# Kernel tuning notes

Hardware: AMD Instinct MI355X
Metric: run time of the kernel (lower is better)

The kernel has to match this reference:

```python
import jax, jax.numpy as jnp
import numpy as np

DIM, NH, HD = 1536, 12, 128
F, H, W = 1, 30, 52
SEQ = F * H * W          # 1560 tokens per AR group
NG, GI = 6, 5            # num_groups, group_idx (attend over full prefix)
POS, EPS = 1024, 1e-6


def _rope_table():
    # cos/sin table matching Wan rope_params: bands [c-2(c//3), c//3, c//3] of head_dim//2
    c = HD // 2
    parts = [c - 2 * (c // 3), c // 3, c // 3]
    pos = np.arange(POS, dtype=np.float64)
    angs = []
    for cp in parts:
        inv = 1.0 / (10000.0 ** (np.arange(cp, dtype=np.float64) / cp))
        angs.append(pos[:, None] * inv[None, :])
    ang = np.concatenate(angs, axis=1)  # [POS, c]
    return jnp.asarray(np.stack([np.cos(ang), np.sin(ang)], axis=-1), dtype=jnp.float32)


def setup_inputs() -> dict:
    key = jax.random.key(0)
    ks = jax.random.split(key, 8)
    lin = lambda k: jax.random.normal(k, (DIM, DIM), jnp.float32) * 0.02
    total = NG * SEQ
    return {
        'x': jax.random.normal(ks[0], (1, SEQ, DIM), jnp.float32),
        'wq': lin(ks[1]), 'bq': jnp.zeros((DIM,), jnp.float32),
        'wk': lin(ks[2]), 'bk': jnp.zeros((DIM,), jnp.float32),
        'wv': lin(ks[3]), 'bv': jnp.zeros((DIM,), jnp.float32),
        'wo': lin(ks[4]), 'bo': jnp.zeros((DIM,), jnp.float32),
        'nq_w': jnp.ones((DIM,), jnp.float32),
        'nk_w': jnp.ones((DIM,), jnp.float32),
        'freqs': _rope_table(),
        'k_cache': jax.random.normal(ks[5], (1, total, NH, HD), jnp.float32) * 0.5,
        'v_cache': jax.random.normal(ks[6], (1, total, NH, HD), jnp.float32) * 0.5,
        'f': F, 'h': H, 'w': W, 'group_idx': GI, 'num_groups': NG,
    }


def _rms_norm(x, weight, eps=EPS):
    # fast_rms_norm: normalize over the full channel dim, then scale
    x = x.astype(jnp.float32)
    return x * jax.lax.rsqrt(jnp.mean(x * x, axis=-1, keepdims=True) + eps) * weight


def _rope_apply(x, freqs, f, h, w, group_idx):
    # x: [B, S, N, D] with S = f*h*w; freqs: [POS, D//2, 2] (cos, sin)
    B, S, N, D = x.shape
    c = D // 2
    cf = c - 2 * (c // 3)
    ch = cw = c // 3
    sf = group_idx * f
    fp = jnp.broadcast_to(freqs[sf:sf + f, :cf][:, None, None], (f, h, w, cf, 2))
    hp = jnp.broadcast_to(freqs[:h, cf:cf + ch][None, :, None], (f, h, w, ch, 2))
    wp = jnp.broadcast_to(freqs[:w, cf + ch:][None, None, :], (f, h, w, cw, 2))
    rot = jnp.concatenate([fp, hp, wp], axis=3).reshape(S, c, 2)  # [S, c, 2]
    cos = rot[..., 0][None, :, None]  # [1, S, 1, c]
    sin = rot[..., 1][None, :, None]
    xr = x.astype(jnp.float32).reshape(B, S, N, c, 2)
    out_r = xr[..., 0] * cos - xr[..., 1] * sin  # complex multiply x * e^{i theta}
    out_i = xr[..., 0] * sin + xr[..., 1] * cos
    return jnp.stack([out_r, out_i], axis=-1).reshape(B, S, N, D)


def reference(x, wq, bq, wk, bk, wv, bv, wo, bo, nq_w, nk_w, freqs,
              k_cache, v_cache, f, h, w, group_idx, num_groups):
    B, S, C = x.shape
    n, d = NH, C // NH
    q = _rms_norm(x @ wq.T + bq, nq_w).reshape(B, S, n, d)
    k = _rms_norm(x @ wk.T + bk, nk_w).reshape(B, S, n, d)
    v = (x @ wv.T + bv).reshape(B, S, n, d)
    q = _rope_apply(q, freqs, f, h, w, group_idx)
    k = _rope_apply(k, freqs, f, h, w, group_idx)
    # KV-cache scatter (detached in the original) then prefix gather
    start = group_idx * S
    kc = jax.lax.dynamic_update_slice(k_cache, jax.lax.stop_gradient(k), (0, start, 0, 0))
    vc = jax.lax.dynamic_update_slice(v_cache, jax.lax.stop_gradient(v), (0, start, 0, 0))
    k_full = kc[:, :start + S]  # [B, Lkv, n, d]
    v_full = vc[:, :start + S]
    att = jnp.einsum('bqnd,bknd->bnqk', q, k_full) / jnp.sqrt(jnp.float32(d))
    p = jax.nn.softmax(att, axis=-1)
    o = jnp.einsum('bnqk,bknd->bqnd', p, v_full).reshape(B, S, C)
    return o @ wo.T + bo
```

## Files before the change

### kernel.cpp

```cpp
#include <hip/hip_runtime.h>

#define DIM 1536
#define NH 12
#define HD 128
#define KSPLIT 8
#define KT 32
#define MFIX 3.0f

typedef _Float16 half2_t __attribute__((ext_vector_type(2)));
typedef _Float16 half8_t __attribute__((ext_vector_type(8)));
typedef float f32x4 __attribute__((ext_vector_type(4)));

__device__ __forceinline__ half2_t pkrtz(float a, float b) {
    return __builtin_bit_cast(half2_t, __builtin_amdgcn_cvt_pkrtz(a, b));
}

__device__ __forceinline__ void split8(float4 a, float4 b, half8_t& h, half8_t& l) {
    half2_t h0 = pkrtz(a.x, a.y), h1 = pkrtz(a.z, a.w);
    half2_t h2 = pkrtz(b.x, b.y), h3 = pkrtz(b.z, b.w);
    half2_t g0 = pkrtz(a.x - (float)h0.x, a.y - (float)h0.y);
    half2_t g1 = pkrtz(a.z - (float)h1.x, a.w - (float)h1.y);
    half2_t g2 = pkrtz(b.x - (float)h2.x, b.y - (float)h2.y);
    half2_t g3 = pkrtz(b.z - (float)h3.x, b.w - (float)h3.y);
    h[0]=h0.x; h[1]=h0.y; h[2]=h1.x; h[3]=h1.y; h[4]=h2.x; h[5]=h2.y; h[6]=h3.x; h[7]=h3.y;
    l[0]=g0.x; l[1]=g0.y; l[2]=g1.x; l[3]=g1.y; l[4]=g2.x; l[5]=g2.y; l[6]=g3.x; l[7]=g3.y;
}

__device__ __forceinline__ half8_t cvt8rn(float4 a, float4 b) {
    half8_t h;
    h[0]=(_Float16)a.x; h[1]=(_Float16)a.y; h[2]=(_Float16)a.z; h[3]=(_Float16)a.w;
    h[4]=(_Float16)b.x; h[5]=(_Float16)b.y; h[6]=(_Float16)b.z; h[7]=(_Float16)b.w;
    return h;
}

__device__ __forceinline__ void gl2lds16(const void* g, void* l) {
    __builtin_amdgcn_global_load_lds(
        (const __attribute__((address_space(1))) unsigned int*)g,
        (__attribute__((address_space(3))) unsigned int*)(unsigned int)(uintptr_t)l,
        16, 0, 0);
}

__global__ __launch_bounds__(256) void cvt_hl(
    const float* __restrict__ src, _Float16* __restrict__ h, _Float16* __restrict__ l, int n8)
{
    const int i = blockIdx.x * 256 + threadIdx.x;
    if (i >= n8) return;
    const float4* s = (const float4*)src + (size_t)i * 2;
    float4 a = s[0], b = s[1];
    half8_t hh, ll; split8(a, b, hh, ll);
    ((half8_t*)h)[i] = hh;
    ((half8_t*)l)[i] = ll;
}

__global__ __launch_bounds__(256) void cvt_hl4(
    const float* __restrict__ s0, const float* __restrict__ s1,
    const float* __restrict__ s2, const float* __restrict__ s3,
    _Float16* __restrict__ h0, _Float16* __restrict__ l0,
    _Float16* __restrict__ h1, _Float16* __restrict__ l1,
    _Float16* __restrict__ h2, _Float16* __restrict__ l2,
    _Float16* __restrict__ h3, _Float16* __restrict__ l3, int n8)
{
    const int i = blockIdx.x * 256 + threadIdx.x;
    if (i >= n8) return;
    const int m = blockIdx.y;
    const float* src = m == 0 ? s0 : m == 1 ? s1 : m == 2 ? s2 : s3;
    _Float16* h = m == 0 ? h0 : m == 1 ? h1 : m == 2 ? h2 : h3;
    _Float16* l = m == 0 ? l0 : m == 1 ? l1 : m == 2 ? l2 : l3;
    const float4* s = (const float4*)src + (size_t)i * 2;
    float4 a = s[0], b = s[1];
    half8_t hh, ll; split8(a, b, hh, ll);
    ((half8_t*)h)[i] = hh;
    ((half8_t*)l)[i] = ll;
}

#define ASTR 40
__global__ __launch_bounds__(256) void gemm_f16_tn(
    const _Float16* __restrict__ Ah, const _Float16* __restrict__ Al,
    const _Float16* __restrict__ Bh0, const _Float16* __restrict__ Bl0,
    const _Float16* __restrict__ Bh1, const _Float16* __restrict__ Bl1,
    const _Float16* __restrict__ Bh2, const _Float16* __restrict__ Bl2,
    const float* __restrict__ bias0, const float* __restrict__ bias1, const float* __restrict__ bias2,
    float* __restrict__ C0, float* __restrict__ C1, float* __restrict__ C2,
    int M)
{
    __shared__ __align__(16) _Float16 AhL[128][ASTR], AlL[128][ASTR];
    __shared__ __align__(16) _Float16 BhL[128][ASTR], BlL[128][ASTR];
    const int bx = blockIdx.x, by = blockIdx.y;
    const int mat = bx / 12, nt = bx % 12;
    const _Float16* Bh   = mat == 0 ? Bh0 : mat == 1 ? Bh1 : Bh2;
    const _Float16* Bl   = mat == 0 ? Bl0 : mat == 1 ? Bl1 : Bl2;
    const float*    bias = mat == 0 ? bias0 : mat == 1 ? bias1 : bias2;
    float*          C    = mat == 0 ? C0 : mat == 1 ? C1 : C2;
    const int m0 = by * 128, n0 = nt * 128;
    const int tid = threadIdx.x;
    const int lane = tid & 63, wave = tid >> 6;
    const int l16 = lane & 15, quad = lane >> 4;
    const int wm = (wave >> 1) * 64, wn = (wave & 1) * 64;
    const int srow = tid >> 1;
    const int scol = (tid & 1) * 16;
    const bool avalid = (m0 + srow) < M;
    const _Float16* ahp = Ah + (size_t)(avalid ? m0 + srow : 0) * DIM + scol;
    const _Float16* alp = Al + (size_t)(avalid ? m0 + srow : 0) * DIM + scol;
    const _Float16* bhp = Bh + (size_t)(n0 + srow) * DIM + scol;
    const _Float16* blp = Bl + (size_t)(n0 + srow) * DIM + scol;

    f32x4 acc[4][4];
    #pragma unroll
    for (int i = 0; i < 4; ++i)
        #pragma unroll
        for (int j = 0; j < 4; ++j) acc[i][j] = (f32x4){0.f, 0.f, 0.f, 0.f};

    for (int kk = 0; kk < DIM; kk += 32) {
        __syncthreads();
        uint4 z = {0, 0, 0, 0};
        uint4 a0 = z, a1 = z, a2 = z, a3 = z;
        if (avalid) {
            a0 = *(const uint4*)(ahp + kk);
            a1 = *(const uint4*)(ahp + kk + 8);
            a2 = *(const uint4*)(alp + kk);
            a3 = *(const uint4*)(alp + kk + 8);
        }
        uint4 b0 = *(const uint4*)(bhp + kk);
        uint4 b1 = *(const uint4*)(bhp + kk + 8);
        uint4 b2 = *(const uint4*)(blp + kk);
        uint4 b3 = *(const uint4*)(blp + kk + 8);
        *(uint4*)&AhL[srow][scol]     = a0;
        *(uint4*)&AhL[srow][scol + 8] = a1;
        *(uint4*)&AlL[srow][scol]     = a2;
        *(uint4*)&AlL[srow][scol + 8] = a3;
        *(uint4*)&BhL[srow][scol]     = b0;
        *(uint4*)&BhL[srow][scol + 8] = b1;
        *(uint4*)&BlL[srow][scol]     = b2;
        *(uint4*)&BlL[srow][scol + 8] = b3;
        __syncthreads();
        half8_t ah[4], al[4], bh[4], bl[4];
        #pragma unroll
        for (int ms = 0; ms < 4; ++ms) {
            ah[ms] = *(const half8_t*)&AhL[wm + ms*16 + l16][quad*8];
            al[ms] = *(const half8_t*)&AlL[wm + ms*16 + l16][quad*8];
        }
        #pragma unroll
        for (int ns = 0; ns < 4; ++ns) {
            bh[ns] = *(const half8_t*)&BhL[wn + ns*16 + l16][quad*8];
            bl[ns] = *(const half8_t*)&BlL[wn + ns*16 + l16][quad*8];
        }
        #pragma unroll
        for (int ms = 0; ms < 4; ++ms)
            #pragma unroll
            for (int ns = 0; ns < 4; ++ns) {
                acc[ms][ns] = __builtin_amdgcn_mfma_f32_16x16x32_f16(ah[ms], bh[ns], acc[ms][ns], 0, 0, 0);
                acc[ms][ns] = __builtin_amdgcn_mfma_f32_16x16x32_f16(ah[ms], bl[ns], acc[ms][ns], 0, 0, 0);
                acc[ms][ns] = __builtin_amdgcn_mfma_f32_16x16x32_f16(al[ms], bh[ns], acc[ms][ns], 0, 0, 0);
            }
    }
    float bv[4];
    #pragma unroll
    for (int ns = 0; ns < 4; ++ns) bv[ns] = bias[n0 + wn + ns*16 + l16];
    #pragma unroll
    for (int ms = 0; ms < 4; ++ms)
        #pragma unroll
        for (int r = 0; r < 4; ++r) {
            const int row = m0 + wm + ms*16 + quad*4 + r;
            if (row < M) {
                #pragma unroll
                for (int ns = 0; ns < 4; ++ns)
                    C[(size_t)row * DIM + n0 + wn + ns*16 + l16] = acc[ms][ns][r] + bv[ns];
            }
        }
}

__global__ __launch_bounds__(256) void rms_rope2(
    float* __restrict__ qb, float* __restrict__ kb,
    const float* __restrict__ wq_, const float* __restrict__ wk_,
    const float* __restrict__ freqs,
    const int* __restrict__ fp, const int* __restrict__ hp,
    const int* __restrict__ wp, const int* __restrict__ gip)
{
    const int s = blockIdx.x;
    float* xv = blockIdx.y ? kb : qb;
    const float* w = blockIdx.y ? wk_ : wq_;
    const int tid = threadIdx.x;
    float* row = xv + (size_t)s * DIM;
    float ss = 0.f;
    for (int c = tid; c < DIM; c += 256) { float v = row[c]; ss += v * v; }
    #pragma unroll
    for (int off = 32; off > 0; off >>= 1) ss += __shfl_down(ss, off, 64);
    __shared__ float red[4];
    if ((tid & 63) == 0) red[tid >> 6] = ss;
    __syncthreads();
    const float tot = red[0] + red[1] + red[2] + red[3];
    const float scale = rsqrtf(tot / (float)DIM + 1e-6f);
    const int f = *fp, h = *hp, ww = *wp, gi = *gip;
    const int hw = h * ww;
    const int fi = s / hw;
    const int rem = s - fi * hw;
    const int hi = rem / ww;
    const int wi = rem - hi * ww;
    const int sf = gi * f;
    for (int p = tid; p < DIM / 2; p += 256) {
        int n = p >> 6, i = p & 63;
        int pos = (i < 22) ? (sf + fi) : (i < 43) ? hi : wi;
        float cs = freqs[pos * 128 + i * 2];
        float sn = freqs[pos * 128 + i * 2 + 1];
        int base = n * HD + 2 * i;
        float x0 = row[base] * scale * w[base];
        float x1 = row[base + 1] * scale * w[base + 1];
        row[base] = x0 * cs - x1 * sn;
        row[base + 1] = x0 * sn + x1 * cs;
    }
}

__global__ __launch_bounds__(256) void kv_prep(
    const float* __restrict__ kws, const float* __restrict__ kcache,
    const float* __restrict__ vws, const float* __restrict__ vcache,
    _Float16* __restrict__ KV, int S, int NT, const int* __restrict__ gip)
{
    const int t = blockIdx.x, n = blockIdx.y;
    const int tid = threadIdx.x;
    const int lane = tid & 63;
    const int l16 = lane & 15, quad = lane >> 4;
    const int start = gip[0] * S;
    const int nk = start + S;
    _Float16* outk = KV + (size_t)(n * NT + t) * 8192;
    _Float16* outv = outk + 4096;
    #pragma unroll
    for (int fi = 0; fi < 2; ++fi) {
        const int f = (tid >> 6) + fi * 4;
        const int ks = f >> 2, db = f & 3;
        const int j = t * KT + ks * 16 + l16;
        float4 a = make_float4(0,0,0,0), b = a;
        if (j < nk) {
            const float* src = (j < start) ? (kcache + (size_t)j * DIM)
                                           : (kws + (size_t)(j - start) * DIM);
            src += n * HD + db * 32 + quad * 8;
            a = *(const float4*)src;
            b = *(const float4*)(src + 4);
        }
        *(half8_t*)&outk[(f * 64 + lane) * 8] = cvt8rn(a, b);
    }
    #pragma unroll
    for (int fi = 0; fi < 2; ++fi) {
        const int ds = (tid >> 6) + fi * 4;
        const int dim = n * HD + ds * 16 + l16;
        half8_t h;
        #pragma unroll
        for (int j = 0; j < 8; ++j) {
            const int key = t * KT + quad * 8 + j;
            float v = 0.f;
            if (key < nk)
                v = (key < start) ? vcache[(size_t)key * DIM + dim]
                                  : vws[(size_t)(key - start) * DIM + dim];
            h[j] = (_Float16)v;
        }
        *(half8_t*)&outv[(ds * 64 + lane) * 8] = h;
    }
}

#define PSTRH 40
__global__ __launch_bounds__(512) void attn_mfma(
    const float* __restrict__ q,
    const _Float16* __restrict__ KV,
    float* __restrict__ Op, float* __restrict__ Ml,
    int S, int NT, const int* __restrict__ gip)
{
    __shared__ __align__(16) _Float16 T[2][8192];
    __shared__ __align__(16) _Float16 Ph[8][16][PSTRH];

    const int nwg = gridDim.x;
    const int L = blockIdx.x;
    const int q8 = nwg >> 3, r8 = nwg & 7;
    const int xcd = L & 7, si = L >> 3;
    const int logical = (xcd < r8 ? xcd * (q8 + 1)
                                  : r8 * (q8 + 1) + (xcd - r8) * q8) + si;
    const int yb = (S + 127) >> 7;
    const int y = logical % yb;
    const int g = logical / yb;
    const int n = g % NH;
    const int ksp = g / NH;
    const int q0 = y * 128;

    const int tid = threadIdx.x;
    const int wave = tid >> 6;
    const int lane = tid & 63;
    const int l16 = lane & 15;
    const int quad = lane >> 4;
    const int start = gip[0] * S;
    const int nk = start + S;
    const int totTiles = (nk + KT - 1) / KT;
    const int tilesPer = (totTiles + KSPLIT - 1) / KSPLIT;
    const int t0 = ksp * tilesPer;
    const int t1 = min(t0 + tilesPer, totTiles);
    const float sc = 0.08838834764831845f;

    half8_t qf[4];
    {
        const int qrow = q0 + wave * 16 + l16;
        const bool qv = qrow < S;
        const float* qp = q + (size_t)(qv ? qrow : 0) * DIM + n * HD + quad * 8;
        #pragma unroll
        for (int db = 0; db < 4; ++db) {
            float4 a = make_float4(0,0,0,0), b = a;
            if (qv) { a = *(const float4*)(qp + db * 32); b = *(const float4*)(qp + db * 32 + 4); }
            qf[db] = cvt8rn(a, b);
        }
    }

    half8_t ones_f;
    {
        _Float16 ov = (l16 == 0) ? (_Float16)1.0f : (_Float16)0.0f;
        #pragma unroll
        for (int j = 0; j < 8; ++j) ones_f[j] = ov;
    }

    f32x4 O[9];
    #pragma unroll
    for (int ds = 0; ds < 9; ++ds) O[ds] = (f32x4){0.f, 0.f, 0.f, 0.f};

    const size_t tb = (size_t)n * NT;

    if (t0 < t1) {
        const _Float16* gp = KV + (tb + t0) * 8192 + wave * 512 + lane * 8;
        gl2lds16(gp,        &T[0][wave * 512]);
        gl2lds16(gp + 4096, &T[0][wave * 512 + 4096]);
    }

    int cur = 0;
    for (int t = t0; t < t1; ++t) {
        if (t + 1 < t1) {
            const _Float16* gp = KV + (tb + t + 1) * 8192 + wave * 512 + lane * 8;
            _Float16* d = &T[cur ^ 1][wave * 512];
            gl2lds16(gp,        d);
            gl2lds16(gp + 4096, d + 4096);
            asm volatile("s_waitcnt vmcnt(2)" ::: "memory");
        } else {
            asm volatile("s_waitcnt vmcnt(0)" ::: "memory");
        }
        __builtin_amdgcn_s_barrier();
        __builtin_amdgcn_sched_barrier(0);

        f32x4 sacc[2];
        sacc[0] = (f32x4){0.f, 0.f, 0.f, 0.f};
        sacc[1] = (f32x4){0.f, 0.f, 0.f, 0.f};
        const half8_t* kh8 = (const half8_t*)&T[cur][0];
        __builtin_amdgcn_s_setprio(1);
        #pragma unroll
        for (int ks = 0; ks < 2; ++ks) {
            #pragma unroll
            for (int db = 0; db < 4; ++db) {
                half8_t bh = kh8[(ks * 4 + db) * 64 + lane];
                sacc[ks] = __builtin_amdgcn_mfma_f32_16x16x32_f16(qf[db], bh, sacc[ks], 0, 0, 0);
            }
        }
        __builtin_amdgcn_s_setprio(0);

        const int k0 = t * KT;
        const bool v0 = (k0 + l16) < nk;
        const bool v1 = (k0 + 16 + l16) < nk;
        #pragma unroll
        for (int r = 0; r < 4; ++r) {
            float p0 = v0 ? __expf(sacc[0][r] * sc - MFIX) : 0.f;
            float p1 = v1 ? __expf(sacc[1][r] * sc - MFIX) : 0.f;
            Ph[wave][quad * 4 + r][l16] = (_Float16)p0;
            Ph[wave][quad * 4 + r][16 + l16] = (_Float16)p1;
        }

        half8_t ph = *(const half8_t*)&Ph[wave][l16][quad * 8];

        const half8_t* vt8 = (const half8_t*)&T[cur][4096];
        __builtin_amdgcn_s_setprio(1);
        #pragma unroll
        for (int ds = 0; ds < 8; ++ds) {
            half8_t vh = vt8[ds * 64 + lane];
            O[ds] = __builtin_amdgcn_mfma_f32_16x16x32_f16(ph, vh, O[ds], 0, 0, 0);
        }
        O[8] = __builtin_amdgcn_mfma_f32_16x16x32_f16(ph, ones_f, O[8], 0, 0, 0);
        __builtin_amdgcn_s_setprio(0);

        __builtin_amdgcn_sched_barrier(0);
        __builtin_amdgcn_s_barrier();
        cur ^= 1;
    }

    #pragma unroll
    for (int r = 0; r < 4; ++r) {
        const int row = q0 + wave * 16 + quad * 4 + r;
        if (row < S) {
            float* op = Op + (((size_t)ksp * NH + n) * S + row) * HD + l16;
            #pragma unroll
            for (int ds = 0; ds < 8; ++ds) op[ds * 16] = O[ds][r];
            if (l16 == 0)
                Ml[((size_t)ksp * NH + n) * S + row] = O[8][r];
        }
    }
}

__global__ __launch_bounds__(256) void attn_merge(
    const float* __restrict__ Op, const float* __restrict__ Ml,
    _Float16* __restrict__ oh, _Float16* __restrict__ ol, int S)
{
    const int idx = blockIdx.x * 256 + threadIdx.x;
    const int total = NH * S * HD / 2;
    if (idx >= total) return;
    const int d0 = (idx & 63) * 2;
    const int t = idx >> 6;
    const int row = t % S;
    const int n = t / S;
    float num0 = 0.f, num1 = 0.f, den = 0.f;
    #pragma unroll
    for (int ks = 0; ks < KSPLIT; ++ks) {
        const size_t base = ((size_t)ks * NH + n) * S + row;
        num0 += Op[base * HD + d0];
        num1 += Op[base * HD + d0 + 1];
        den += Ml[base];
    }
    const float v0 = num0 / den, v1 = num1 / den;
    half2_t h = pkrtz(v0, v1);
    half2_t l = pkrtz(v0 - (float)h.x, v1 - (float)h.y);
    const size_t oidx = (size_t)row * DIM + n * HD + d0;
    *(half2_t*)&oh[oidx] = h;
    *(half2_t*)&ol[oidx] = l;
}

extern "C" void kernel_launch(void* const* d_in, const int* in_sizes, int n_in,
                              void* d_out, int out_size, void* d_ws, size_t ws_size,
                              hipStream_t stream)
{
    const float* x      = (const float*)d_in[0];
    const float* wq     = (const float*)d_in[1];
    const float* bq     = (const float*)d_in[2];
    const float* wk     = (const float*)d_in[3];
    const float* bk     = (const float*)d_in[4];
    const float* wv     = (const float*)d_in[5];
    const float* bv     = (const float*)d_in[6];
    const float* wo     = (const float*)d_in[7];
    const float* bo     = (const float*)d_in[8];
    const float* nqw    = (const float*)d_in[9];
    const float* nkw    = (const float*)d_in[10];
    const float* freqs  = (const float*)d_in[11];
    const float* kcache = (const float*)d_in[12];
    const float* vcache = (const float*)d_in[13];
    const int*   fp     = (const int*)d_in[14];
    const int*   hp     = (const int*)d_in[15];
    const int*   wp     = (const int*)d_in[16];
    const int*   gip    = (const int*)d_in[17];

    const int S = in_sizes[0] / DIM;
    const int total = in_sizes[12] / (NH * HD);
    const int NT = (total + KT - 1) / KT;
    const size_t sd = (size_t)S * DIM;
    const size_t wsz = (size_t)DIM * DIM;

    char* p = (char*)d_ws;
    float* q  = (float*)p;            p += sd * 4;
    float* k  = (float*)p;            p += sd * 4;
    float* v  = (float*)p;            p += sd * 4;
    float* Op = (float*)p;            p += (size_t)KSPLIT * NH * S * HD * 4;
    float* Ml = (float*)p;            p += (size_t)KSPLIT * NH * S * 4;
    _Float16* KV  = (_Float16*)p;     p += (size_t)NH * NT * 8192 * 2;
    _Float16* xh  = (_Float16*)p;     p += sd * 2;
    _Float16* xl  = (_Float16*)p;     p += sd * 2;
    _Float16* oh  = (_Float16*)p;     p += sd * 2;
    _Float16* ol  = (_Float16*)p;     p += sd * 2;
    _Float16* wqh = (_Float16*)p;     p += wsz * 2;
    _Float16* wql = (_Float16*)p;     p += wsz * 2;
    _Float16* wkh = (_Float16*)p;     p += wsz * 2;
    _Float16* wkl = (_Float16*)p;     p += wsz * 2;
    _Float16* wvh = (_Float16*)p;     p += wsz * 2;
    _Float16* wvl = (_Float16*)p;     p += wsz * 2;
    _Float16* woh = (_Float16*)p;     p += wsz * 2;
    _Float16* wol = (_Float16*)p;     p += wsz * 2;
    float* out = (float*)d_out;

    const int mt = (S + 127) / 128;
    const int xn8 = (int)(sd / 8), wn8 = (int)(wsz / 8);

    cvt_hl<<<dim3((xn8 + 255) / 256), dim3(256), 0, stream>>>(x, xh, xl, xn8);
    cvt_hl4<<<dim3((wn8 + 255) / 256, 4), dim3(256), 0, stream>>>(
        wq, wk, wv, wo, wqh, wql, wkh, wkl, wvh, wvl, woh, wol, wn8);

    gemm_f16_tn<<<dim3(36, mt), dim3(256), 0, stream>>>(
        xh, xl, wqh, wql, wkh, wkl, wvh, wvl, bq, bk, bv, q, k, v, S);
    rms_rope2<<<dim3(S, 2), dim3(256), 0, stream>>>(q, k, nqw, nkw, freqs, fp, hp, wp, gip);
    kv_prep<<<dim3(NT, NH), dim3(256), 0, stream>>>(k, kcache, v, vcache, KV, S, NT, gip);
    {
        const int yb = (S + 127) / 128;
        const int nwg = NH * yb * KSPLIT;
        attn_mfma<<<dim3(nwg), dim3(512), 0, stream>>>(
            q, KV, Op, Ml, S, NT, gip);
    }
    attn_merge<<<dim3((NH * S * HD / 2 + 255) / 256), dim3(256), 0, stream>>>(Op, Ml, oh, ol, S);
    gemm_f16_tn<<<dim3(12, mt), dim3(256), 0, stream>>>(
        oh, ol, woh, wol, woh, wol, woh, wol, bo, bo, bo, out, out, out, S);
}
```

Measured before the change: 518.3 us.

## Pre-tile GEMM operands into MFMA fragment layout with async double-buffered LDS loads

The fp16 hi/lo conversion kernels and the attention merge now write activations and weights in a tiled, fragment-ordered layout, one 4096-element record per 128x32 tile. The GEMM can then stage each tile with direct global-to-LDS 16-byte loads, double-buffered with explicit vmcnt waits and raw barriers, and read fragments from LDS without padding. Blocks are also remapped across XCDs, and MFMA priority is raised with setprio. This is meant to cut register-staged load overhead and to overlap global loads with MFMA work. The cost is padded workspace for the M tail and a more fragile layout contract between kernels.

```diff
diff --git a/kernel.cpp b/kernel.cpp
--- a/kernel.cpp
+++ b/kernel.cpp
@@ -6,6 +6,7 @@
 #define KSPLIT 8
 #define KT 32
 #define MFIX 3.0f
+#define KK48 48
 
 typedef _Float16 half2_t __attribute__((ext_vector_type(2)));
 typedef _Float16 half8_t __attribute__((ext_vector_type(8)));
@@ -40,41 +41,57 @@
         16, 0, 0);
 }
 
-__global__ __launch_bounds__(256) void cvt_hl(
-    const float* __restrict__ src, _Float16* __restrict__ h, _Float16* __restrict__ l, int n8)
+
+__global__ __launch_bounds__(256) void cvt_a_fl(
+    const float* __restrict__ src, _Float16* __restrict__ h, _Float16* __restrict__ l,
+    int M, int nrec8)
 {
     const int i = blockIdx.x * 256 + threadIdx.x;
-    if (i >= n8) return;
-    const float4* s = (const float4*)src + (size_t)i * 2;
-    float4 a = s[0], b = s[1];
+    if (i >= nrec8) return;
+    const int lane = i & 63;
+    const int grp  = (i >> 6) & 7;
+    const int tile = i >> 9;
+    const int kk = tile % KK48, mt = tile / KK48;
+    const int row = mt * 128 + grp * 16 + (lane & 15);
+    const int k   = kk * 32 + (lane >> 4) * 8;
+    float4 a = make_float4(0,0,0,0), b = a;
+    if (row < M) {
+        const float* s = src + (size_t)row * DIM + k;
+        a = *(const float4*)s; b = *(const float4*)(s + 4);
+    }
     half8_t hh, ll; split8(a, b, hh, ll);
     ((half8_t*)h)[i] = hh;
     ((half8_t*)l)[i] = ll;
 }
 
-__global__ __launch_bounds__(256) void cvt_hl4(
+__global__ __launch_bounds__(256) void cvt_w_fl(
     const float* __restrict__ s0, const float* __restrict__ s1,
     const float* __restrict__ s2, const float* __restrict__ s3,
     _Float16* __restrict__ h0, _Float16* __restrict__ l0,
     _Float16* __restrict__ h1, _Float16* __restrict__ l1,
     _Float16* __restrict__ h2, _Float16* __restrict__ l2,
-    _Float16* __restrict__ h3, _Float16* __restrict__ l3, int n8)
+    _Float16* __restrict__ h3, _Float16* __restrict__ l3, int nrec8)
 {
     const int i = blockIdx.x * 256 + threadIdx.x;
-    if (i >= n8) return;
+    if (i >= nrec8) return;
     const int m = blockIdx.y;
     const float* src = m == 0 ? s0 : m == 1 ? s1 : m == 2 ? s2 : s3;
     _Float16* h = m == 0 ? h0 : m == 1 ? h1 : m == 2 ? h2 : h3;
     _Float16* l = m == 0 ? l0 : m == 1 ? l1 : m == 2 ? l2 : l3;
-    const float4* s = (const float4*)src + (size_t)i * 2;
-    float4 a = s[0], b = s[1];
+    const int lane = i & 63;
+    const int grp  = (i >> 6) & 7;
+    const int tile = i >> 9;
+    const int kk = tile % KK48, nt = tile / KK48;
+    const int row = nt * 128 + grp * 16 + (lane & 15);
+    const int k   = kk * 32 + (lane >> 4) * 8;
+    const float* s = src + (size_t)row * DIM + k;
+    float4 a = *(const float4*)s, b = *(const float4*)(s + 4);
     half8_t hh, ll; split8(a, b, hh, ll);
     ((half8_t*)h)[i] = hh;
     ((half8_t*)l)[i] = ll;
 }
 
-#define ASTR 40
-__global__ __launch_bounds__(256) void gemm_f16_tn(
+__global__ __launch_bounds__(256) void gemm_fl(
     const _Float16* __restrict__ Ah, const _Float16* __restrict__ Al,
     const _Float16* __restrict__ Bh0, const _Float16* __restrict__ Bl0,
     const _Float16* __restrict__ Bh1, const _Float16* __restrict__ Bl1,
@@ -83,26 +100,33 @@
     float* __restrict__ C0, float* __restrict__ C1, float* __restrict__ C2,
     int M)
 {
-    __shared__ __align__(16) _Float16 AhL[128][ASTR], AlL[128][ASTR];
-    __shared__ __align__(16) _Float16 BhL[128][ASTR], BlL[128][ASTR];
-    const int bx = blockIdx.x, by = blockIdx.y;
-    const int mat = bx / 12, nt = bx % 12;
+    __shared__ __align__(16) _Float16 T[2][4][4096];
+
+    const int MT = (M + 127) >> 7;
+    const int nwg = gridDim.x;
+    const int L = blockIdx.x;
+    const int q8 = nwg >> 3, r8 = nwg & 7;
+    const int xcd = L & 7, si = L >> 3;
+    const int logical = (xcd < r8 ? xcd * (q8 + 1)
+                                  : r8 * (q8 + 1) + (xcd - r8) * q8) + si;
+    const int bxx = logical / MT;
+    const int myy = logical % MT;
+    const int mat = bxx / 12, nt = bxx % 12;
     const _Float16* Bh   = mat == 0 ? Bh0 : mat == 1 ? Bh1 : Bh2;
     const _Float16* Bl   = mat == 0 ? Bl0 : mat == 1 ? Bl1 : Bl2;
     const float*    bias = mat == 0 ? bias0 : mat == 1 ? bias1 : bias2;
     float*          C    = mat == 0 ? C0 : mat == 1 ? C1 : C2;
-    const int m0 = by * 128, n0 = nt * 128;
+    const int m0 = myy * 128, n0 = nt * 128;
+
     const int tid = threadIdx.x;
     const int lane = tid & 63, wave = tid >> 6;
     const int l16 = lane & 15, quad = lane >> 4;
     const int wm = (wave >> 1) * 64, wn = (wave & 1) * 64;
-    const int srow = tid >> 1;
-    const int scol = (tid & 1) * 16;
-    const bool avalid = (m0 + srow) < M;
-    const _Float16* ahp = Ah + (size_t)(avalid ? m0 + srow : 0) * DIM + scol;
-    const _Float16* alp = Al + (size_t)(avalid ? m0 + srow : 0) * DIM + scol;
-    const _Float16* bhp = Bh + (size_t)(n0 + srow) * DIM + scol;
-    const _Float16* blp = Bl + (size_t)(n0 + srow) * DIM + scol;
+
+    const _Float16* Arh = Ah + (size_t)myy * KK48 * 4096;
+    const _Float16* Arl = Al + (size_t)myy * KK48 * 4096;
+    const _Float16* Brh = Bh + (size_t)nt  * KK48 * 4096;
+    const _Float16* Brl = Bl + (size_t)nt  * KK48 * 4096;
 
     f32x4 acc[4][4];
     #pragma unroll
@@ -110,40 +134,50 @@
         #pragma unroll
         for (int j = 0; j < 4; ++j) acc[i][j] = (f32x4){0.f, 0.f, 0.f, 0.f};
 
-    for (int kk = 0; kk < DIM; kk += 32) {
-        __syncthreads();
-        uint4 z = {0, 0, 0, 0};
-        uint4 a0 = z, a1 = z, a2 = z, a3 = z;
-        if (avalid) {
-            a0 = *(const uint4*)(ahp + kk);
-            a1 = *(const uint4*)(ahp + kk + 8);
-            a2 = *(const uint4*)(alp + kk);
-            a3 = *(const uint4*)(alp + kk + 8);
-        }
-        uint4 b0 = *(const uint4*)(bhp + kk);
-        uint4 b1 = *(const uint4*)(bhp + kk + 8);
-        uint4 b2 = *(const uint4*)(blp + kk);
-        uint4 b3 = *(const uint4*)(blp + kk + 8);
-        *(uint4*)&AhL[srow][scol]     = a0;
-        *(uint4*)&AhL[srow][scol + 8] = a1;
-        *(uint4*)&AlL[srow][scol]     = a2;
-        *(uint4*)&AlL[srow][scol + 8] = a3;
-        *(uint4*)&BhL[srow][scol]     = b0;
-        *(uint4*)&BhL[srow][scol + 8] = b1;
-        *(uint4*)&BlL[srow][scol]     = b2;
-        *(uint4*)&BlL[srow][scol + 8] = b3;
-        __syncthreads();
+    auto STAGE = [&](int kk, int buf) {
+        const size_t off = (size_t)kk * 4096 + wave * 1024 + lane * 8;
+        _Float16* d0 = &T[buf][0][wave * 1024];
+        _Float16* d1 = &T[buf][1][wave * 1024];
+        _Float16* d2 = &T[buf][2][wave * 1024];
+        _Float16* d3 = &T[buf][3][wave * 1024];
+        gl2lds16(Arh + off,       d0);
+        gl2lds16(Arh + off + 512, d0 + 512);
+        gl2lds16(Arl + off,       d1);
+        gl2lds16(Arl + off + 512, d1 + 512);
+        gl2lds16(Brh + off,       d2);
+        gl2lds16(Brh + off + 512, d2 + 512);
+        gl2lds16(Brl + off,       d3);
+        gl2lds16(Brl + off + 512, d3 + 512);
+    };
+
+    STAGE(0, 0);
+    int cur = 0;
+    for (int kk = 0; kk < KK48; ++kk) {
+        if (kk + 1 < KK48) {
+            STAGE(kk + 1, cur ^ 1);
+            asm volatile("s_waitcnt vmcnt(8)" ::: "memory");
+        } else {
+            asm volatile("s_waitcnt vmcnt(0)" ::: "memory");
+        }
+        __builtin_amdgcn_s_barrier();
+        __builtin_amdgcn_sched_barrier(0);
+
         half8_t ah[4], al[4], bh[4], bl[4];
+        const half8_t* tA = (const half8_t*)&T[cur][0][0];
+        const half8_t* tAl= (const half8_t*)&T[cur][1][0];
+        const half8_t* tB = (const half8_t*)&T[cur][2][0];
+        const half8_t* tBl= (const half8_t*)&T[cur][3][0];
         #pragma unroll
         for (int ms = 0; ms < 4; ++ms) {
-            ah[ms] = *(const half8_t*)&AhL[wm + ms*16 + l16][quad*8];
-            al[ms] = *(const half8_t*)&AlL[wm + ms*16 + l16][quad*8];
+            ah[ms] = tA [((wm >> 4) + ms) * 64 + lane];
+            al[ms] = tAl[((wm >> 4) + ms) * 64 + lane];
         }
         #pragma unroll
         for (int ns = 0; ns < 4; ++ns) {
-            bh[ns] = *(const half8_t*)&BhL[wn + ns*16 + l16][quad*8];
-            bl[ns] = *(const half8_t*)&BlL[wn + ns*16 + l16][quad*8];
-        }
+            bh[ns] = tB [((wn >> 4) + ns) * 64 + lane];
+            bl[ns] = tBl[((wn >> 4) + ns) * 64 + lane];
+        }
+        __builtin_amdgcn_s_setprio(1);
         #pragma unroll
         for (int ms = 0; ms < 4; ++ms)
             #pragma unroll
@@ -152,7 +186,13 @@
                 acc[ms][ns] = __builtin_amdgcn_mfma_f32_16x16x32_f16(ah[ms], bl[ns], acc[ms][ns], 0, 0, 0);
                 acc[ms][ns] = __builtin_amdgcn_mfma_f32_16x16x32_f16(al[ms], bh[ns], acc[ms][ns], 0, 0, 0);
             }
-    }
+        __builtin_amdgcn_s_setprio(0);
+
+        __builtin_amdgcn_sched_barrier(0);
+        __builtin_amdgcn_s_barrier();
+        cur ^= 1;
+    }
+
     float bv[4];
     #pragma unroll
     for (int ns = 0; ns < 4; ++ns) bv[ns] = bias[n0 + wn + ns*16 + l16];
@@ -416,9 +456,14 @@
     const float v0 = num0 / den, v1 = num1 / den;
     half2_t h = pkrtz(v0, v1);
     half2_t l = pkrtz(v0 - (float)h.x, v1 - (float)h.y);
-    const size_t oidx = (size_t)row * DIM + n * HD + d0;
-    *(half2_t*)&oh[oidx] = h;
-    *(half2_t*)&ol[oidx] = l;
+    const int k = n * HD + d0;
+    const int mt = row >> 7, rr = row & 127;
+    const int grp = rr >> 4, l16r = rr & 15;
+    const int kk = k >> 5, quad = (k & 31) >> 3, jj = k & 7;
+    const size_t a = ((size_t)(mt * KK48 + kk) * 4096)
+                   + ((size_t)(grp * 64 + quad * 16 + l16r) * 8) + jj;
+    *(half2_t*)&oh[a] = h;
+    *(half2_t*)&ol[a] = l;
 }
 
 extern "C" void kernel_launch(void* const* d_in, const int* in_sizes, int n_in,
@@ -447,8 +492,10 @@
     const int S = in_sizes[0] / DIM;
     const int total = in_sizes[12] / (NH * HD);
     const int NT = (total + KT - 1) / KT;
+    const int MT = (S + 127) / 128;
     const size_t sd = (size_t)S * DIM;
-    const size_t wsz = (size_t)DIM * DIM;
+    const size_t arec = (size_t)MT * KK48 * 4096;
+    const size_t wrec = (size_t)12 * KK48 * 4096;
 
     char* p = (char*)d_ws;
     float* q  = (float*)p;            p += sd * 4;
@@ -457,28 +504,27 @@
     float* Op = (float*)p;            p += (size_t)KSPLIT * NH * S * HD * 4;
     float* Ml = (float*)p;            p += (size_t)KSPLIT * NH * S * 4;
     _Float16* KV  = (_Float16*)p;     p += (size_t)NH * NT * 8192 * 2;
-    _Float16* xh  = (_Float16*)p;     p += sd * 2;
-    _Float16* xl  = (_Float16*)p;     p += sd * 2;
-    _Float16* oh  = (_Float16*)p;     p += sd * 2;
-    _Float16* ol  = (_Float16*)p;     p += sd * 2;
-    _Float16* wqh = (_Float16*)p;     p += wsz * 2;
-    _Float16* wql = (_Float16*)p;     p += wsz * 2;
-    _Float16* wkh = (_Float16*)p;     p += wsz * 2;
-    _Float16* wkl = (_Float16*)p;     p += wsz * 2;
-    _Float16* wvh = (_Float16*)p;     p += wsz * 2;
-    _Float16* wvl = (_Float16*)p;     p += wsz * 2;
-    _Float16* woh = (_Float16*)p;     p += wsz * 2;
-    _Float16* wol = (_Float16*)p;     p += wsz * 2;
+    _Float16* xh  = (_Float16*)p;     p += arec * 2;
+    _Float16* xl  = (_Float16*)p;     p += arec * 2;
+    _Float16* oh  = (_Float16*)p;     p += arec * 2;
+    _Float16* ol  = (_Float16*)p;     p += arec * 2;
+    _Float16* wqh = (_Float16*)p;     p += wrec * 2;
+    _Float16* wql = (_Float16*)p;     p += wrec * 2;
+    _Float16* wkh = (_Float16*)p;     p += wrec * 2;
+    _Float16* wkl = (_Float16*)p;     p += wrec * 2;
+    _Float16* wvh = (_Float16*)p;     p += wrec * 2;
+    _Float16* wvl = (_Float16*)p;     p += wrec * 2;
+    _Float16* woh = (_Float16*)p;     p += wrec * 2;
+    _Float16* wol = (_Float16*)p;     p += wrec * 2;
     float* out = (float*)d_out;
 
-    const int mt = (S + 127) / 128;
-    const int xn8 = (int)(sd / 8), wn8 = (int)(wsz / 8);
-
-    cvt_hl<<<dim3((xn8 + 255) / 256), dim3(256), 0, stream>>>(x, xh, xl, xn8);
-    cvt_hl4<<<dim3((wn8 + 255) / 256, 4), dim3(256), 0, stream>>>(
+    const int an8 = (int)(arec / 8), wn8 = (int)(wrec / 8);
+
+    cvt_a_fl<<<dim3((an8 + 255) / 256), dim3(256), 0, stream>>>(x, xh, xl, S, an8);
+    cvt_w_fl<<<dim3((wn8 + 255) / 256, 4), dim3(256), 0, stream>>>(
         wq, wk, wv, wo, wqh, wql, wkh, wkl, wvh, wvl, woh, wol, wn8);
 
-    gemm_f16_tn<<<dim3(36, mt), dim3(256), 0, stream>>>(
+    gemm_fl<<<dim3(36 * MT), dim3(256), 0, stream>>>(
         xh, xl, wqh, wql, wkh, wkl, wvh, wvl, bq, bk, bv, q, k, v, S);
     rms_rope2<<<dim3(S, 2), dim3(256), 0, stream>>>(q, k, nqw, nkw, freqs, fp, hp, wp, gip);
     kv_prep<<<dim3(NT, NH), dim3(256), 0, stream>>>(k, kcache, v, vcache, KV, S, NT, gip);
@@ -489,6 +535,6 @@
             q, KV, Op, Ml, S, NT, gip);
     }
     attn_merge<<<dim3((NH * S * HD / 2 + 255) / 256), dim3(256), 0, stream>>>(Op, Ml, oh, ol, S);
-    gemm_f16_tn<<<dim3(12, mt), dim3(256), 0, stream>>>(
+    gemm_fl<<<dim3(12 * MT), dim3(256), 0, stream>>>(
         oh, ol, woh, wol, woh, wol, woh, wol, bo, bo, bo, out, out, out, S);
 }
```

New measurement: 473.8 us. 8.6% less time.
